# Performance work log

Measured on AMD Instinct MI355X. Metric: run time of the kernel, lower is better.

Reference implementation:

```python
import jax, jax.numpy as jnp
import numpy as np

NUM_NODES = 8192
NUM_EDGES = 262144
IN_C = 512
OUT_C = 512


def setup_inputs() -> dict:
    key = jax.random.key(0)
    k1, k2, k3, k4 = jax.random.split(key, 4)
    x = jax.random.normal(k1, (NUM_NODES, IN_C), dtype=jnp.float32)
    edge_index = jax.random.randint(k2, (2, NUM_EDGES), 0, NUM_NODES, dtype=jnp.int64)
    # nn.Linear params (W: [out, in], b: [out]) with kaiming-ish scale
    W = jax.random.normal(k3, (OUT_C, IN_C), dtype=jnp.float32) * (1.0 / np.sqrt(IN_C))
    b = jax.random.normal(k4, (OUT_C,), dtype=jnp.float32) * 0.01
    return {"x": x, "edge_index": edge_index, "W": W, "b": b}


def reference(x, edge_index, W, b):
    n = x.shape[0]
    # append self loops
    loop = jnp.arange(n, dtype=edge_index.dtype)
    rows = jnp.concatenate([edge_index[0], loop])
    cols = jnp.concatenate([edge_index[1], loop])
    # dense adjacency via scatter-set (duplicates collapse to 1.0, matching torch indexing assign)
    adj = jnp.zeros((n, n), dtype=jnp.float32).at[rows, cols].set(1.0)
    deg = adj.sum(axis=1)
    deg_inv_sqrt = jnp.where(deg > 0, jax.lax.rsqrt(jnp.maximum(deg, 1e-30)), 0.0)
    norm = deg_inv_sqrt[:, None] * adj * deg_inv_sqrt[None, :]
    h = x @ W.T + b            # [N, out_c]
    return norm @ h            # [N, out_c]
```

## Files before the change

### kernel.cpp

```cpp
#include <hip/hip_runtime.h>
#include <stdint.h>

#define N_NODES 8192
#define N_EDGES 262144
#define IN_C    512
#define OUT_C   512
#define MAX_DEG 512

typedef __attribute__((ext_vector_type(8))) short short8;
typedef __attribute__((ext_vector_type(4))) float f32x4;

__device__ inline uint16_t f2bf(float f) {
    uint32_t u = __float_as_uint(f);
    uint32_t r = (u + 0x7FFFu + ((u >> 16) & 1u)) >> 16;
    return (uint16_t)r;
}

__global__ void f32_to_bf16_k(const float* __restrict__ in, uint16_t* __restrict__ out, int n) {
    int i = (blockIdx.x * 256 + threadIdx.x) * 4;
    if (i >= n) return;
    float4 v = *(const float4*)(in + i);
    ushort4 o;
    o.x = f2bf(v.x); o.y = f2bf(v.y); o.z = f2bf(v.z); o.w = f2bf(v.w);
    *(ushort4*)(out + i) = o;
}

__global__ void build_graph_k(const int* __restrict__ ei, uint32_t* __restrict__ bitmap,
                              int* __restrict__ cnt, uint16_t* __restrict__ nbr) {
    int t = blockIdx.x * blockDim.x + threadIdx.x;
    int r, c;
    if (t < N_EDGES) {
        r = ei[t];
        c = ei[N_EDGES + t];
    } else if (t < N_EDGES + N_NODES) {
        r = t - N_EDGES; c = r;
    } else return;
    uint32_t bitidx = (uint32_t)r * N_NODES + (uint32_t)c;
    uint32_t word = bitidx >> 5;
    uint32_t mask = 1u << (bitidx & 31u);
    uint32_t old = atomicOr(&bitmap[word], mask);
    if (!(old & mask)) {
        int pos = atomicAdd(&cnt[r], 1);
        if (pos < MAX_DEG) nbr[r * MAX_DEG + pos] = (uint16_t)c;
    }
}

__global__ __launch_bounds__(256) void gemm_hb_k(const uint16_t* __restrict__ xb,
                                                 const uint16_t* __restrict__ wb,
                                                 const float* __restrict__ bias,
                                                 uint16_t* __restrict__ h) {
    const int wave = threadIdx.x >> 6;
    const int lane = threadIdx.x & 63;
    const int quad = lane >> 4;
    const int l16  = lane & 15;
    const int m_base = blockIdx.y * 256 + wave * 64;
    const int n_base = blockIdx.x * 64;

    f32x4 acc[4][4];
    #pragma unroll
    for (int a = 0; a < 4; a++)
        #pragma unroll
        for (int s = 0; s < 4; s++) acc[a][s] = (f32x4){0.f, 0.f, 0.f, 0.f};

    for (int k0 = 0; k0 < IN_C; k0 += 32) {
        short8 af[4], bf[4];
        #pragma unroll
        for (int a = 0; a < 4; a++)
            af[a] = *(const short8*)(xb + (m_base + a * 16 + l16) * IN_C + quad * 8 + k0);
        #pragma unroll
        for (int s = 0; s < 4; s++)
            bf[s] = *(const short8*)(wb + (n_base + s * 16 + l16) * IN_C + quad * 8 + k0);
        #pragma unroll
        for (int a = 0; a < 4; a++)
            #pragma unroll
            for (int s = 0; s < 4; s++)
                acc[a][s] = __builtin_amdgcn_mfma_f32_16x16x32_bf16(af[a], bf[s], acc[a][s], 0, 0, 0);
    }
    #pragma unroll
    for (int s = 0; s < 4; s++) {
        int col = n_base + s * 16 + l16;
        float bv = bias[col];
        #pragma unroll
        for (int a = 0; a < 4; a++) {
            int row = m_base + a * 16 + quad * 4;
            #pragma unroll
            for (int r = 0; r < 4; r++)
                h[(row + r) * OUT_C + col] = f2bf(acc[a][s][r] + bv);
        }
    }
}

__global__ __launch_bounds__(128) void aggregate_k(const int* __restrict__ cnt,
                                                   const uint16_t* __restrict__ nbr,
                                                   const uint32_t* __restrict__ h2,
                                                   float* __restrict__ out) {
    const int i = blockIdx.x;
    const int half = blockIdx.y;
    int m = cnt[i]; if (m > MAX_DEG) m = MAX_DEG;

    __shared__ uint16_t jl[MAX_DEG];
    __shared__ float    dl[MAX_DEG];
    for (int t = threadIdx.x; t < m; t += 128) {
        uint16_t j = nbr[i * MAX_DEG + t];
        jl[t] = j;
        dl[t] = rsqrtf((float)cnt[j]);
    }
    __syncthreads();

    const uint32_t* hp = h2 + half * 128 + threadIdx.x;
    float s0 = 0.f, s1 = 0.f;
    for (int l = 0; l < m; l++) {
        uint32_t u = hp[(int)jl[l] * 256];
        float dj = dl[l];
        s0 += dj * __uint_as_float(u << 16);
        s1 += dj * __uint_as_float(u & 0xFFFF0000u);
    }
    float di = rsqrtf((float)m);
    int c = half * 256 + threadIdx.x * 2;
    float2 o = {di * s0, di * s1};
    *(float2*)(out + i * OUT_C + c) = o;
}

extern "C" void kernel_launch(void* const* d_in, const int* in_sizes, int n_in,
                              void* d_out, int out_size, void* d_ws, size_t ws_size,
                              hipStream_t stream) {
    const float* x  = (const float*)d_in[0];
    const int*   ei = (const int*)  d_in[1];
    const float* W  = (const float*)d_in[2];
    const float* b  = (const float*)d_in[3];
    float* out = (float*)d_out;
    char* ws = (char*)d_ws;

    const size_t BITMAP_OFF = 0;
    const size_t CNT_OFF    = 8388608;
    const size_t NBR_OFF    = CNT_OFF + 32768;
    const size_t XB_OFF     = NBR_OFF + 8388608;
    const size_t WB_OFF     = XB_OFF + 8388608;
    const size_t H_OFF      = WB_OFF + 524288;
    uint32_t* bitmap = (uint32_t*)(ws + BITMAP_OFF);
    int*      cnt    = (int*)     (ws + CNT_OFF);
    uint16_t* nbr    = (uint16_t*)(ws + NBR_OFF);
    uint16_t* xb     = (uint16_t*)(ws + XB_OFF);
    uint16_t* wb     = (uint16_t*)(ws + WB_OFF);
    uint16_t* h      = (uint16_t*)(ws + H_OFF);

    hipMemsetAsync(bitmap, 0, 8388608, stream);
    hipMemsetAsync(cnt, 0, 32768, stream);

    f32_to_bf16_k<<<(N_NODES * IN_C / 4 + 255) / 256, 256, 0, stream>>>(x, xb, N_NODES * IN_C);
    f32_to_bf16_k<<<(OUT_C * IN_C / 4 + 255) / 256, 256, 0, stream>>>(W, wb, OUT_C * IN_C);

    build_graph_k<<<(N_EDGES + N_NODES + 255) / 256, 256, 0, stream>>>(ei, bitmap, cnt, nbr);

    gemm_hb_k<<<dim3(OUT_C / 64, N_NODES / 256), 256, 0, stream>>>(xb, wb, b, h);

    aggregate_k<<<dim3(N_NODES, 2), 128, 0, stream>>>(cnt, nbr, (const uint32_t*)h, out);
}
```

Measured before the change: 147.9 us.

## Merge conversion launches and memsets, retile GEMM waves, unroll aggregation loop

Folds the x and W bf16 conversions into a single launch that handles 8 elements per thread, and clears the bitmap and count buffers with one memset since they are contiguous. The GEMM tile changes so each block covers 128x64 with waves arranged 2x2 (64x32 each), doubling the block count to improve occupancy, though each wave now reuses its A fragments across fewer B columns. The aggregation loop gets unroll 4 so more gather loads can be in flight. These are several small independent changes aimed at launch overhead and latency.

```diff
diff --git a/kernel.cpp b/kernel.cpp
--- a/kernel.cpp
+++ b/kernel.cpp
@@ -6,6 +6,8 @@
 #define IN_C    512
 #define OUT_C   512
 #define MAX_DEG 512
+#define X_ELEMS (N_NODES * IN_C)
+#define W_ELEMS (OUT_C * IN_C)
 
 typedef __attribute__((ext_vector_type(8))) short short8;
 typedef __attribute__((ext_vector_type(4))) float f32x4;
@@ -16,17 +18,27 @@
     return (uint16_t)r;
 }
 
-__global__ void f32_to_bf16_k(const float* __restrict__ in, uint16_t* __restrict__ out, int n) {
-    int i = (blockIdx.x * 256 + threadIdx.x) * 4;
-    if (i >= n) return;
-    float4 v = *(const float4*)(in + i);
-    ushort4 o;
-    o.x = f2bf(v.x); o.y = f2bf(v.y); o.z = f2bf(v.z); o.w = f2bf(v.w);
-    *(ushort4*)(out + i) = o;
+__global__ __launch_bounds__(256) void convert_k(const float* __restrict__ x,
+                                                 const float* __restrict__ W,
+                                                 uint16_t* __restrict__ xb,
+                                                 uint16_t* __restrict__ wb) {
+    int i = (blockIdx.x * 256 + threadIdx.x) * 8;
+    const float* src; uint16_t* dst;
+    if (i < X_ELEMS) { src = x + i; dst = xb + i; }
+    else             { src = W + (i - X_ELEMS); dst = wb + (i - X_ELEMS); }
+    float4 v0 = *(const float4*)(src);
+    float4 v1 = *(const float4*)(src + 4);
+    ushort4 o0, o1;
+    o0.x = f2bf(v0.x); o0.y = f2bf(v0.y); o0.z = f2bf(v0.z); o0.w = f2bf(v0.w);
+    o1.x = f2bf(v1.x); o1.y = f2bf(v1.y); o1.z = f2bf(v1.z); o1.w = f2bf(v1.w);
+    *(ushort4*)(dst)     = o0;
+    *(ushort4*)(dst + 4) = o1;
 }
 
-__global__ void build_graph_k(const int* __restrict__ ei, uint32_t* __restrict__ bitmap,
-                              int* __restrict__ cnt, uint16_t* __restrict__ nbr) {
+__global__ __launch_bounds__(256) void build_graph_k(const int* __restrict__ ei,
+                                                     uint32_t* __restrict__ bitmap,
+                                                     int* __restrict__ cnt,
+                                                     uint16_t* __restrict__ nbr) {
     int t = blockIdx.x * blockDim.x + threadIdx.x;
     int r, c;
     if (t < N_EDGES) {
@@ -36,10 +48,8 @@
         r = t - N_EDGES; c = r;
     } else return;
     uint32_t bitidx = (uint32_t)r * N_NODES + (uint32_t)c;
-    uint32_t word = bitidx >> 5;
-    uint32_t mask = 1u << (bitidx & 31u);
-    uint32_t old = atomicOr(&bitmap[word], mask);
-    if (!(old & mask)) {
+    uint32_t old = atomicOr(&bitmap[bitidx >> 5], 1u << (bitidx & 31u));
+    if (!(old & (1u << (bitidx & 31u)))) {
         int pos = atomicAdd(&cnt[r], 1);
         if (pos < MAX_DEG) nbr[r * MAX_DEG + pos] = (uint16_t)c;
     }
@@ -53,31 +63,31 @@
     const int lane = threadIdx.x & 63;
     const int quad = lane >> 4;
     const int l16  = lane & 15;
-    const int m_base = blockIdx.y * 256 + wave * 64;
-    const int n_base = blockIdx.x * 64;
+    const int m_base = blockIdx.y * 128 + (wave & 1) * 64;
+    const int n_base = blockIdx.x * 64 + (wave >> 1) * 32;
 
-    f32x4 acc[4][4];
+    f32x4 acc[4][2];
     #pragma unroll
     for (int a = 0; a < 4; a++)
         #pragma unroll
-        for (int s = 0; s < 4; s++) acc[a][s] = (f32x4){0.f, 0.f, 0.f, 0.f};
+        for (int s = 0; s < 2; s++) acc[a][s] = (f32x4){0.f, 0.f, 0.f, 0.f};
 
     for (int k0 = 0; k0 < IN_C; k0 += 32) {
-        short8 af[4], bf[4];
+        short8 af[4], bf[2];
         #pragma unroll
         for (int a = 0; a < 4; a++)
             af[a] = *(const short8*)(xb + (m_base + a * 16 + l16) * IN_C + quad * 8 + k0);
         #pragma unroll
-        for (int s = 0; s < 4; s++)
+        for (int s = 0; s < 2; s++)
             bf[s] = *(const short8*)(wb + (n_base + s * 16 + l16) * IN_C + quad * 8 + k0);
         #pragma unroll
         for (int a = 0; a < 4; a++)
             #pragma unroll
-            for (int s = 0; s < 4; s++)
+            for (int s = 0; s < 2; s++)
                 acc[a][s] = __builtin_amdgcn_mfma_f32_16x16x32_bf16(af[a], bf[s], acc[a][s], 0, 0, 0);
     }
     #pragma unroll
-    for (int s = 0; s < 4; s++) {
+    for (int s = 0; s < 2; s++) {
         int col = n_base + s * 16 + l16;
         float bv = bias[col];
         #pragma unroll
@@ -109,6 +119,7 @@
 
     const uint32_t* hp = h2 + half * 128 + threadIdx.x;
     float s0 = 0.f, s1 = 0.f;
+    #pragma unroll 4
     for (int l = 0; l < m; l++) {
         uint32_t u = hp[(int)jl[l] * 256];
         float dj = dl[l];
@@ -144,15 +155,13 @@
     uint16_t* wb     = (uint16_t*)(ws + WB_OFF);
     uint16_t* h      = (uint16_t*)(ws + H_OFF);
 
-    hipMemsetAsync(bitmap, 0, 8388608, stream);
-    hipMemsetAsync(cnt, 0, 32768, stream);
+    hipMemsetAsync(bitmap, 0, 8388608 + 32768, stream);
 
-    f32_to_bf16_k<<<(N_NODES * IN_C / 4 + 255) / 256, 256, 0, stream>>>(x, xb, N_NODES * IN_C);
-    f32_to_bf16_k<<<(OUT_C * IN_C / 4 + 255) / 256, 256, 0, stream>>>(W, wb, OUT_C * IN_C);
+    convert_k<<<(X_ELEMS + W_ELEMS) / (256 * 8), 256, 0, stream>>>(x, W, xb, wb);
 
     build_graph_k<<<(N_EDGES + N_NODES + 255) / 256, 256, 0, stream>>>(ei, bitmap, cnt, nbr);
 
-    gemm_hb_k<<<dim3(OUT_C / 64, N_NODES / 256), 256, 0, stream>>>(xb, wb, b, h);
+    gemm_hb_k<<<dim3(OUT_C / 64, N_NODES / 128), 256, 0, stream>>>(xb, wb, b, h);
 
     aggregate_k<<<dim3(N_NODES, 2), 128, 0, stream>>>(cnt, nbr, (const uint32_t*)h, out);
 }
```

New measurement: 151.6 us. 1.03x slower.
